# Kernel tuning notes

Hardware: AMD Instinct MI355X
Metric: run time of the kernel (lower is better)

## Reference

```python
import jax, jax.numpy as jnp
import numpy as np

TOP_K = 2

def setup_inputs() -> dict:
    key = jax.random.key(0)
    ks = jax.random.split(key, 5)
    B, S, H, F, E = 4, 512, 1024, 3584, 8
    x = jax.random.normal(ks[0], (B, S, H), dtype=jnp.float32)
    gate_w = jax.random.normal(ks[1], (H, E), dtype=jnp.float32) * (1.0 / np.sqrt(H))
    w1 = jax.random.normal(ks[2], (E, F, H), dtype=jnp.float32) * (1.0 / np.sqrt(H))
    w3 = jax.random.normal(ks[3], (E, F, H), dtype=jnp.float32) * (1.0 / np.sqrt(H))
    w2 = jax.random.normal(ks[4], (E, H, F), dtype=jnp.float32) * (1.0 / np.sqrt(F))
    return {"x": x, "gate_w": gate_w, "w1": w1, "w3": w3, "w2": w2}


def reference(x, gate_w, w1, w3, w2):
    # MoE top-2 routing (Mixtral-style), dense-dispatch formulation.
    B, S, H = x.shape
    E = gate_w.shape[1]
    xt = x.reshape(-1, H)                      # [T, H] flattened tokens
    T = xt.shape[0]
    logits = xt @ gate_w                       # [T, E] gate logits
    top_w, top_i = jax.lax.top_k(logits, TOP_K)    # [T, K]
    top_w = jax.nn.softmax(top_w, axis=-1)         # softmax over selected-k logits
    # combine[t, e] = routing weight of expert e for token t (0 if not selected)
    combine = jnp.zeros((T, E), dtype=xt.dtype)
    combine = combine.at[jnp.arange(T)[:, None], top_i].add(top_w)
    # SwiGLU experts: y_e = w2_e @ (silu(w1_e x) * (w3_e x))
    h = jnp.einsum('th,efh->tef', xt, w1)      # [T, E, F]
    g = jnp.einsum('th,efh->tef', xt, w3)      # [T, E, F]
    act = jax.nn.silu(h) * g                   # [T, E, F]
    out_e = jnp.einsum('tef,ehf->teh', act, w2)  # [T, E, H]
    out = jnp.einsum('teh,te->th', out_e, combine)  # weighted combine over experts
    return out.reshape(B, S, H)
```

## Files before the change

kernel.cpp:

```cpp
#include <hip/hip_runtime.h>
#include <hip/hip_bf16.h>
#include <stdint.h>

#define TOKENS 2048
#define HDIM 1024
#define FDIM 3584
#define NEXP 8
#define BK 32

typedef __attribute__((ext_vector_type(8))) short short8;
typedef __attribute__((ext_vector_type(4))) float floatx4;

#define AS1 __attribute__((address_space(1)))
#define AS3 __attribute__((address_space(3)))

__device__ __forceinline__ void glds16(const void* g, void* l) {
  __builtin_amdgcn_global_load_lds((const AS1 void*)g, (AS3 void*)l, 16, 0, 0);
}

__device__ __forceinline__ unsigned short f2bf(float f) {
  union { float f; unsigned int u; } c; c.f = f;
  unsigned int u = c.u;
  u += 0x7fffu + ((u >> 16) & 1u);
  return (unsigned short)(u >> 16);
}

__device__ __forceinline__ unsigned int pk2bf(float a, float b) {
  __hip_bfloat162 h = __float22bfloat162_rn(make_float2(a, b));
  union { __hip_bfloat162 h; unsigned int u; } c; c.h = h;
  return c.u;
}

__device__ __forceinline__ short8 pack_bf16(float4 c0, float4 c1) {
  union { short8 s; uint4 u; } o;
  o.u.x = pk2bf(c0.x, c0.y); o.u.y = pk2bf(c0.z, c0.w);
  o.u.z = pk2bf(c1.x, c1.y); o.u.w = pk2bf(c1.z, c1.w);
  return o.s;
}

__global__ void gate_kernel(const float* __restrict__ x,
                            const float* __restrict__ gw,
                            int* __restrict__ top_e,
                            float* __restrict__ top_w,
                            int* __restrict__ count) {
  int wv = threadIdx.x >> 6;
  int lane = threadIdx.x & 63;
  int t = blockIdx.x * 4 + wv;
  if (t >= TOKENS) return;
  float p[NEXP];
#pragma unroll
  for (int e = 0; e < NEXP; e++) p[e] = 0.f;
  const float* xr = x + (size_t)t * HDIM;
  for (int h = lane; h < HDIM; h += 64) {
    float xv = xr[h];
    const float4* g4 = (const float4*)(gw + (size_t)h * NEXP);
    float4 a = g4[0], b = g4[1];
    p[0] += xv * a.x; p[1] += xv * a.y; p[2] += xv * a.z; p[3] += xv * a.w;
    p[4] += xv * b.x; p[5] += xv * b.y; p[6] += xv * b.z; p[7] += xv * b.w;
  }
#pragma unroll
  for (int e = 0; e < NEXP; e++) {
#pragma unroll
    for (int off = 32; off > 0; off >>= 1) p[e] += __shfl_xor(p[e], off, 64);
  }
  if (lane == 0) {
    int i0 = 0;
    for (int e = 1; e < NEXP; e++) if (p[e] > p[i0]) i0 = e;
    int i1 = (i0 == 0) ? 1 : 0;
    for (int e = 0; e < NEXP; e++) if (e != i0 && p[e] > p[i1]) i1 = e;
    float l0 = p[i0], l1 = p[i1];
    float e1 = __expf(l1 - l0);
    float s = 1.f + e1;
    top_e[t * 2] = i0; top_e[t * 2 + 1] = i1;
    top_w[t * 2] = 1.f / s; top_w[t * 2 + 1] = e1 / s;
    atomicAdd(&count[i0], 1);
    atomicAdd(&count[i1], 1);
  }
}

__global__ void offsets_kernel(const int* __restrict__ count,
                               int* __restrict__ offs,
                               int* __restrict__ cursor) {
  if (threadIdx.x == 0 && blockIdx.x == 0) {
    int o = 0;
    for (int e = 0; e < NEXP; e++) { offs[e] = o; cursor[e] = o; o += count[e]; }
  }
}

__global__ void scatter_kernel(const int* __restrict__ top_e,
                               int* __restrict__ cursor,
                               int* __restrict__ tok_of,
                               int* __restrict__ slot_of) {
  int t = blockIdx.x * blockDim.x + threadIdx.x;
  if (t >= TOKENS) return;
#pragma unroll
  for (int k = 0; k < 2; k++) {
    int e = top_e[t * 2 + k];
    int g = atomicAdd(&cursor[e], 1);
    tok_of[g] = t;
    slot_of[t * 2 + k] = g;
  }
}

__global__ void xconv_kernel(const float* __restrict__ x,
                             unsigned short* __restrict__ xbf) {
  int i = (blockIdx.x * blockDim.x + threadIdx.x) * 4;
  float4 v = *(const float4*)(x + i);
  uint2 pk;
  pk.x = pk2bf(v.x, v.y);
  pk.y = pk2bf(v.z, v.w);
  *(uint2*)(xbf + i) = pk;
}

#define G1_BM 128
#define G1_BF 64

__global__ __launch_bounds__(256, 3)
void gemm1_kernel(const unsigned short* __restrict__ xbf,
                  const float* __restrict__ w1,
                  const float* __restrict__ w3,
                  const int* __restrict__ count,
                  const int* __restrict__ offs,
                  const int* __restrict__ tok_of,
                  unsigned short* __restrict__ act) {
  int e = blockIdx.z;
  int cnt = count[e];
  int m0 = blockIdx.y * G1_BM;
  if (m0 >= cnt) return;
  int f0 = blockIdx.x * G1_BF;
  int off_e = offs[e];

  __shared__ __align__(16) unsigned short sA[G1_BM * 32];
  __shared__ __align__(16) float sB1[G1_BF * 32];
  __shared__ __align__(16) float sB3[G1_BF * 32];

  int tid = threadIdx.x;
  int lane = tid & 63, wv = tid >> 6;

  const unsigned short* ag[2];
  char* alb[2];
  const float* g1p[2]; const float* g3p[2];
  char* blb[2];
#pragma unroll
  for (int p = 0; p < 2; p++) {
    int c = tid + p * 256;
    {
      int row = c >> 2, slot = c & 3;
      int gch = slot ^ ((row >> 1) & 3);
      int r = m0 + row;
      int tok = tok_of[off_e + (r < cnt ? r : 0)];
      ag[p] = xbf + (size_t)tok * HDIM + gch * 8;
      alb[p] = (char*)sA + (wv * 64 + p * 256) * 16;
    }
    {
      int row = c >> 3, slot = c & 7;
      int gch = slot ^ (row & 7);
      g1p[p] = w1 + ((size_t)e * FDIM + f0 + row) * HDIM + gch * 4;
      g3p[p] = w3 + ((size_t)e * FDIM + f0 + row) * HDIM + gch * 4;
      blb[p] = (char*)sB1 + (wv * 64 + p * 256) * 16;
    }
  }
  size_t b3delta = (char*)sB3 - (char*)sB1;

  int lrow = lane & 15, quad = lane >> 4;
  int wm = wv >> 1, wn = wv & 1;

  floatx4 acc1[4][2], acc3[4][2];
#pragma unroll
  for (int i = 0; i < 4; i++)
#pragma unroll
    for (int j = 0; j < 2; j++) {
      acc1[i][j] = (floatx4){0.f, 0.f, 0.f, 0.f};
      acc3[i][j] = (floatx4){0.f, 0.f, 0.f, 0.f};
    }

  for (int k0 = 0; k0 < HDIM; k0 += BK) {
    __syncthreads();
#pragma unroll
    for (int p = 0; p < 2; p++) {
      glds16(ag[p] + k0, alb[p]);
      glds16(g1p[p] + k0, blb[p]);
      glds16(g3p[p] + k0, blb[p] + b3delta);
    }
    __syncthreads();

    short8 af[4], b1f[2], b3f[2];
#pragma unroll
    for (int ms = 0; ms < 4; ms++) {
      int r = wm * 64 + ms * 16 + lrow;
      int sl = quad ^ ((r >> 1) & 3);
      af[ms] = *(const short8*)(sA + r * 32 + sl * 8);
    }
#pragma unroll
    for (int ns = 0; ns < 2; ns++) {
      int r = wn * 32 + ns * 16 + lrow;
      int s0 = (2 * quad) ^ (r & 7), s1 = (2 * quad + 1) ^ (r & 7);
      float4 c0 = *(const float4*)(sB1 + r * 32 + s0 * 4);
      float4 c1 = *(const float4*)(sB1 + r * 32 + s1 * 4);
      b1f[ns] = pack_bf16(c0, c1);
      float4 d0 = *(const float4*)(sB3 + r * 32 + s0 * 4);
      float4 d1 = *(const float4*)(sB3 + r * 32 + s1 * 4);
      b3f[ns] = pack_bf16(d0, d1);
    }
#pragma unroll
    for (int ms = 0; ms < 4; ms++)
#pragma unroll
      for (int ns = 0; ns < 2; ns++) {
        acc1[ms][ns] = __builtin_amdgcn_mfma_f32_16x16x32_bf16(af[ms], b1f[ns], acc1[ms][ns], 0, 0, 0);
        acc3[ms][ns] = __builtin_amdgcn_mfma_f32_16x16x32_bf16(af[ms], b3f[ns], acc3[ms][ns], 0, 0, 0);
      }
  }

#pragma unroll
  for (int ms = 0; ms < 4; ms++) {
#pragma unroll
    for (int reg = 0; reg < 4; reg++) {
      int slot = m0 + wm * 64 + ms * 16 + quad * 4 + reg;
      if (slot < cnt) {
        unsigned short* ar = act + (size_t)(off_e + slot) * FDIM + f0 + wn * 32;
#pragma unroll
        for (int ns = 0; ns < 2; ns++) {
          float h = acc1[ms][ns][reg];
          float g = acc3[ms][ns][reg];
          float a = h / (1.f + __expf(-h)) * g;
          ar[ns * 16 + lrow] = f2bf(a);
        }
      }
    }
  }
}

#define G2_BM 128
#define G2_BN 128
#define SPLITK 4
#define G2_KS (FDIM / SPLITK)

__global__ __launch_bounds__(256, 3)
void gemm2_kernel(const unsigned short* __restrict__ act,
                  const float* __restrict__ w2,
                  const int* __restrict__ count,
                  const int* __restrict__ offs,
                  float* __restrict__ part) {
  int zz = blockIdx.z;
  int e = zz & 7, sk = zz >> 3;
  int cnt = count[e];
  int m0 = blockIdx.y * G2_BM;
  if (m0 >= cnt) return;
  int h0 = blockIdx.x * G2_BN;
  int off_e = offs[e];
  int kb = sk * G2_KS;

  __shared__ __align__(16) unsigned short sA[G2_BM * 32];
  __shared__ __align__(16) float sB[G2_BN * 32];

  int tid = threadIdx.x;
  int lane = tid & 63, wv = tid >> 6;

  const unsigned short* ag[2];
  char* alb[2];
#pragma unroll
  for (int p = 0; p < 2; p++) {
    int c = tid + p * 256;
    int row = c >> 2, slot = c & 3;
    int gch = slot ^ ((row >> 1) & 3);
    int r = m0 + row;
    int rr = (r < cnt ? r : 0);
    ag[p] = act + (size_t)(off_e + rr) * FDIM + kb + gch * 8;
    alb[p] = (char*)sA + (wv * 64 + p * 256) * 16;
  }
  const float* bg[4];
  char* blb[4];
#pragma unroll
  for (int p = 0; p < 4; p++) {
    int c = tid + p * 256;
    int row = c >> 3, slot = c & 7;
    int gch = slot ^ (row & 7);
    bg[p] = w2 + ((size_t)e * HDIM + h0 + row) * FDIM + kb + gch * 4;
    blb[p] = (char*)sB + (wv * 64 + p * 256) * 16;
  }

  int lrow = lane & 15, quad = lane >> 4;
  int wm = wv >> 1, wn = wv & 1;

  floatx4 acc[4][4];
#pragma unroll
  for (int i = 0; i < 4; i++)
#pragma unroll
    for (int j = 0; j < 4; j++) acc[i][j] = (floatx4){0.f, 0.f, 0.f, 0.f};

  for (int k0 = 0; k0 < G2_KS; k0 += BK) {
    __syncthreads();
#pragma unroll
    for (int p = 0; p < 2; p++) glds16(ag[p] + k0, alb[p]);
#pragma unroll
    for (int p = 0; p < 4; p++) glds16(bg[p] + k0, blb[p]);
    __syncthreads();

    short8 af[4], bf[4];
#pragma unroll
    for (int ms = 0; ms < 4; ms++) {
      int r = wm * 64 + ms * 16 + lrow;
      int sl = quad ^ ((r >> 1) & 3);
      af[ms] = *(const short8*)(sA + r * 32 + sl * 8);
    }
#pragma unroll
    for (int ns = 0; ns < 4; ns++) {
      int r = wn * 64 + ns * 16 + lrow;
      int s0 = (2 * quad) ^ (r & 7), s1 = (2 * quad + 1) ^ (r & 7);
      float4 c0 = *(const float4*)(sB + r * 32 + s0 * 4);
      float4 c1 = *(const float4*)(sB + r * 32 + s1 * 4);
      bf[ns] = pack_bf16(c0, c1);
    }
#pragma unroll
    for (int ms = 0; ms < 4; ms++)
#pragma unroll
      for (int ns = 0; ns < 4; ns++)
        acc[ms][ns] = __builtin_amdgcn_mfma_f32_16x16x32_bf16(af[ms], bf[ns], acc[ms][ns], 0, 0, 0);
  }

#pragma unroll
  for (int ms = 0; ms < 4; ms++) {
#pragma unroll
    for (int reg = 0; reg < 4; reg++) {
      int slot = m0 + wm * 64 + ms * 16 + quad * 4 + reg;
      if (slot < cnt) {
        float* crow = part + ((size_t)sk * 4096 + off_e + slot) * HDIM + h0 + wn * 64;
#pragma unroll
        for (int ns = 0; ns < 4; ns++)
          crow[ns * 16 + lrow] = acc[ms][ns][reg];
      }
    }
  }
}

__global__ void combine_kernel(const float* __restrict__ part,
                               const int* __restrict__ slot_of,
                               const float* __restrict__ top_w,
                               float* __restrict__ out) {
  int t = blockIdx.x;
  int g0 = slot_of[t * 2], g1 = slot_of[t * 2 + 1];
  float w0 = top_w[t * 2], w1 = top_w[t * 2 + 1];
  int i = threadIdx.x;
  float4 s0 = {0.f, 0.f, 0.f, 0.f}, s1 = {0.f, 0.f, 0.f, 0.f};
#pragma unroll
  for (int sk = 0; sk < SPLITK; sk++) {
    float4 a = ((const float4*)(part + ((size_t)sk * 4096 + g0) * HDIM))[i];
    float4 b = ((const float4*)(part + ((size_t)sk * 4096 + g1) * HDIM))[i];
    s0.x += a.x; s0.y += a.y; s0.z += a.z; s0.w += a.w;
    s1.x += b.x; s1.y += b.y; s1.z += b.z; s1.w += b.w;
  }
  float4 r;
  r.x = w0 * s0.x + w1 * s1.x;
  r.y = w0 * s0.y + w1 * s1.y;
  r.z = w0 * s0.z + w1 * s1.z;
  r.w = w0 * s0.w + w1 * s1.w;
  ((float4*)(out + (size_t)t * HDIM))[i] = r;
}

extern "C" void kernel_launch(void* const* d_in, const int* in_sizes, int n_in,
                              void* d_out, int out_size, void* d_ws, size_t ws_size,
                              hipStream_t stream) {
  const float* x  = (const float*)d_in[0];
  const float* gw = (const float*)d_in[1];
  const float* w1 = (const float*)d_in[2];
  const float* w3 = (const float*)d_in[3];
  const float* w2 = (const float*)d_in[4];
  float* out = (float*)d_out;

  char* ws = (char*)d_ws;
  const size_t XBF_OFF = 0;
  const size_t ACT_OFF = 4ull << 20;
  const size_t PART_OFF = 36ull << 20;
  const size_t SML_OFF = 100ull << 20;

  unsigned short* xbf = (unsigned short*)(ws + XBF_OFF);
  unsigned short* act = (unsigned short*)(ws + ACT_OFF);
  float* part = (float*)(ws + PART_OFF);
  float* top_w = (float*)(ws + SML_OFF);
  int* top_e   = (int*)(ws + SML_OFF + 16384);
  int* slot_of = (int*)(ws + SML_OFF + 32768);
  int* tok_of  = (int*)(ws + SML_OFF + 49152);
  int* count   = (int*)(ws + SML_OFF + 65536);
  int* offs    = (int*)(ws + SML_OFF + 65536 + 32);
  int* cursor  = (int*)(ws + SML_OFF + 65536 + 64);

  hipMemsetAsync(count, 0, 96, stream);

  gate_kernel<<<TOKENS / 4, 256, 0, stream>>>(x, gw, top_e, top_w, count);
  offsets_kernel<<<1, 64, 0, stream>>>(count, offs, cursor);
  scatter_kernel<<<TOKENS / 256, 256, 0, stream>>>(top_e, cursor, tok_of, slot_of);
  xconv_kernel<<<(TOKENS * HDIM) / (256 * 4), 256, 0, stream>>>(x, xbf);
  gemm1_kernel<<<dim3(FDIM / G1_BF, TOKENS / G1_BM, NEXP), 256, 0, stream>>>(
      xbf, w1, w3, count, offs, tok_of, act);
  gemm2_kernel<<<dim3(HDIM / G2_BN, TOKENS / G2_BM, NEXP * SPLITK), 256, 0, stream>>>(
      act, w2, count, offs, part);
  combine_kernel<<<TOKENS, 256, 0, stream>>>(part, slot_of, top_w, out);
}
```

Measured before the change: 566.7 us.

## Pre-convert expert weights to bf16 and double-buffer LDS tiles in both GEMMs

Adds a pass on every call that converts w1, w3 and w2 from fp32 to bf16 in workspace. Both expert GEMMs then stream half as many bytes from the weights and skip the per-tile fp32-to-bf16 packing in their inner loops. The GEMM main loops are also restructured into two-stage LDS double buffering with a single barrier per K step, and launch bounds are raised to 4 blocks per CU. The trade-off is an extra full read and write of all weights each call, plus a larger workspace layout in which the partial-sum buffer reuses the w1/w3 bf16 region once those are no longer needed.

```diff
diff --git a/kernel.cpp b/kernel.cpp
--- a/kernel.cpp
+++ b/kernel.cpp
@@ -29,13 +29,6 @@
   __hip_bfloat162 h = __float22bfloat162_rn(make_float2(a, b));
   union { __hip_bfloat162 h; unsigned int u; } c; c.h = h;
   return c.u;
-}
-
-__device__ __forceinline__ short8 pack_bf16(float4 c0, float4 c1) {
-  union { short8 s; uint4 u; } o;
-  o.u.x = pk2bf(c0.x, c0.y); o.u.y = pk2bf(c0.z, c0.w);
-  o.u.z = pk2bf(c1.x, c1.y); o.u.w = pk2bf(c1.z, c1.w);
-  return o.s;
 }
 
 __global__ void gate_kernel(const float* __restrict__ x,
@@ -112,13 +105,36 @@
   *(uint2*)(xbf + i) = pk;
 }
 
+#define WELEMS 29360128
+#define WBLK (WELEMS / 2048)
+
+__global__ void wconv_kernel(const float* __restrict__ w1,
+                             const float* __restrict__ w3,
+                             const float* __restrict__ w2,
+                             unsigned short* __restrict__ w1b,
+                             unsigned short* __restrict__ w3b,
+                             unsigned short* __restrict__ w2b) {
+  int b = blockIdx.x;
+  const float* src; unsigned short* dst;
+  if (b < WBLK) { src = w1; dst = w1b; }
+  else if (b < 2 * WBLK) { src = w3; dst = w3b; b -= WBLK; }
+  else { src = w2; dst = w2b; b -= 2 * WBLK; }
+  size_t i = ((size_t)b * 256 + threadIdx.x) * 8;
+  float4 v0 = *(const float4*)(src + i);
+  float4 v1 = *(const float4*)(src + i + 4);
+  uint4 o;
+  o.x = pk2bf(v0.x, v0.y); o.y = pk2bf(v0.z, v0.w);
+  o.z = pk2bf(v1.x, v1.y); o.w = pk2bf(v1.z, v1.w);
+  *(uint4*)(dst + i) = o;
+}
+
 #define G1_BM 128
 #define G1_BF 64
 
-__global__ __launch_bounds__(256, 3)
+__global__ __launch_bounds__(256, 4)
 void gemm1_kernel(const unsigned short* __restrict__ xbf,
-                  const float* __restrict__ w1,
-                  const float* __restrict__ w3,
+                  const unsigned short* __restrict__ w1b,
+                  const unsigned short* __restrict__ w3b,
                   const int* __restrict__ count,
                   const int* __restrict__ offs,
                   const int* __restrict__ tok_of,
@@ -130,37 +146,30 @@
   int f0 = blockIdx.x * G1_BF;
   int off_e = offs[e];
 
-  __shared__ __align__(16) unsigned short sA[G1_BM * 32];
-  __shared__ __align__(16) float sB1[G1_BF * 32];
-  __shared__ __align__(16) float sB3[G1_BF * 32];
+  __shared__ __align__(16) unsigned short sA[2][G1_BM * 32];
+  __shared__ __align__(16) unsigned short sB1[2][G1_BF * 32];
+  __shared__ __align__(16) unsigned short sB3[2][G1_BF * 32];
 
   int tid = threadIdx.x;
   int lane = tid & 63, wv = tid >> 6;
 
   const unsigned short* ag[2];
-  char* alb[2];
-  const float* g1p[2]; const float* g3p[2];
-  char* blb[2];
 #pragma unroll
   for (int p = 0; p < 2; p++) {
     int c = tid + p * 256;
-    {
-      int row = c >> 2, slot = c & 3;
-      int gch = slot ^ ((row >> 1) & 3);
-      int r = m0 + row;
-      int tok = tok_of[off_e + (r < cnt ? r : 0)];
-      ag[p] = xbf + (size_t)tok * HDIM + gch * 8;
-      alb[p] = (char*)sA + (wv * 64 + p * 256) * 16;
-    }
-    {
-      int row = c >> 3, slot = c & 7;
-      int gch = slot ^ (row & 7);
-      g1p[p] = w1 + ((size_t)e * FDIM + f0 + row) * HDIM + gch * 4;
-      g3p[p] = w3 + ((size_t)e * FDIM + f0 + row) * HDIM + gch * 4;
-      blb[p] = (char*)sB1 + (wv * 64 + p * 256) * 16;
-    }
-  }
-  size_t b3delta = (char*)sB3 - (char*)sB1;
+    int row = c >> 2, slot = c & 3;
+    int gch = slot ^ ((row >> 1) & 3);
+    int r = m0 + row;
+    int tok = tok_of[off_e + (r < cnt ? r : 0)];
+    ag[p] = xbf + (size_t)tok * HDIM + gch * 8;
+  }
+  unsigned aoff = (unsigned)(wv * 64) * 16;
+
+  int brow = tid >> 2, bslot = tid & 3;
+  int bgch = bslot ^ ((brow >> 1) & 3);
+  const unsigned short* b1g = w1b + ((size_t)e * FDIM + f0 + brow) * HDIM + bgch * 8;
+  const unsigned short* b3g = w3b + ((size_t)e * FDIM + f0 + brow) * HDIM + bgch * 8;
+  unsigned boff = (unsigned)(wv * 64) * 16;
 
   int lrow = lane & 15, quad = lane >> 4;
   int wm = wv >> 1, wn = wv & 1;
@@ -174,33 +183,38 @@
       acc3[i][j] = (floatx4){0.f, 0.f, 0.f, 0.f};
     }
 
+#pragma unroll
+  for (int p = 0; p < 2; p++)
+    glds16(ag[p], (char*)sA[0] + aoff + p * 4096);
+  glds16(b1g, (char*)sB1[0] + boff);
+  glds16(b3g, (char*)sB3[0] + boff);
+  __syncthreads();
+
+  int cur = 0;
   for (int k0 = 0; k0 < HDIM; k0 += BK) {
-    __syncthreads();
-#pragma unroll
-    for (int p = 0; p < 2; p++) {
-      glds16(ag[p] + k0, alb[p]);
-      glds16(g1p[p] + k0, blb[p]);
-      glds16(g3p[p] + k0, blb[p] + b3delta);
-    }
-    __syncthreads();
+    int kn = k0 + BK;
+    if (kn < HDIM) {
+      int nxt = cur ^ 1;
+#pragma unroll
+      for (int p = 0; p < 2; p++)
+        glds16(ag[p] + kn, (char*)sA[nxt] + aoff + p * 4096);
+      glds16(b1g + kn, (char*)sB1[nxt] + boff);
+      glds16(b3g + kn, (char*)sB3[nxt] + boff);
+    }
 
     short8 af[4], b1f[2], b3f[2];
 #pragma unroll
     for (int ms = 0; ms < 4; ms++) {
       int r = wm * 64 + ms * 16 + lrow;
       int sl = quad ^ ((r >> 1) & 3);
-      af[ms] = *(const short8*)(sA + r * 32 + sl * 8);
+      af[ms] = *(const short8*)(sA[cur] + r * 32 + sl * 8);
     }
 #pragma unroll
     for (int ns = 0; ns < 2; ns++) {
       int r = wn * 32 + ns * 16 + lrow;
-      int s0 = (2 * quad) ^ (r & 7), s1 = (2 * quad + 1) ^ (r & 7);
-      float4 c0 = *(const float4*)(sB1 + r * 32 + s0 * 4);
-      float4 c1 = *(const float4*)(sB1 + r * 32 + s1 * 4);
-      b1f[ns] = pack_bf16(c0, c1);
-      float4 d0 = *(const float4*)(sB3 + r * 32 + s0 * 4);
-      float4 d1 = *(const float4*)(sB3 + r * 32 + s1 * 4);
-      b3f[ns] = pack_bf16(d0, d1);
+      int sl = quad ^ ((r >> 1) & 3);
+      b1f[ns] = *(const short8*)(sB1[cur] + r * 32 + sl * 8);
+      b3f[ns] = *(const short8*)(sB3[cur] + r * 32 + sl * 8);
     }
 #pragma unroll
     for (int ms = 0; ms < 4; ms++)
@@ -209,6 +223,8 @@
         acc1[ms][ns] = __builtin_amdgcn_mfma_f32_16x16x32_bf16(af[ms], b1f[ns], acc1[ms][ns], 0, 0, 0);
         acc3[ms][ns] = __builtin_amdgcn_mfma_f32_16x16x32_bf16(af[ms], b3f[ns], acc3[ms][ns], 0, 0, 0);
       }
+    __syncthreads();
+    cur ^= 1;
   }
 
 #pragma unroll
@@ -235,9 +251,9 @@
 #define SPLITK 4
 #define G2_KS (FDIM / SPLITK)
 
-__global__ __launch_bounds__(256, 3)
+__global__ __launch_bounds__(256, 4)
 void gemm2_kernel(const unsigned short* __restrict__ act,
-                  const float* __restrict__ w2,
+                  const unsigned short* __restrict__ w2b,
                   const int* __restrict__ count,
                   const int* __restrict__ offs,
                   float* __restrict__ part) {
@@ -250,34 +266,27 @@
   int off_e = offs[e];
   int kb = sk * G2_KS;
 
-  __shared__ __align__(16) unsigned short sA[G2_BM * 32];
-  __shared__ __align__(16) float sB[G2_BN * 32];
+  __shared__ __align__(16) unsigned short sA[2][G2_BM * 32];
+  __shared__ __align__(16) unsigned short sB[2][G2_BN * 32];
 
   int tid = threadIdx.x;
   int lane = tid & 63, wv = tid >> 6;
 
   const unsigned short* ag[2];
-  char* alb[2];
+  const unsigned short* bg[2];
 #pragma unroll
   for (int p = 0; p < 2; p++) {
     int c = tid + p * 256;
     int row = c >> 2, slot = c & 3;
     int gch = slot ^ ((row >> 1) & 3);
-    int r = m0 + row;
-    int rr = (r < cnt ? r : 0);
-    ag[p] = act + (size_t)(off_e + rr) * FDIM + kb + gch * 8;
-    alb[p] = (char*)sA + (wv * 64 + p * 256) * 16;
-  }
-  const float* bg[4];
-  char* blb[4];
-#pragma unroll
-  for (int p = 0; p < 4; p++) {
-    int c = tid + p * 256;
-    int row = c >> 3, slot = c & 7;
-    int gch = slot ^ (row & 7);
-    bg[p] = w2 + ((size_t)e * HDIM + h0 + row) * FDIM + kb + gch * 4;
-    blb[p] = (char*)sB + (wv * 64 + p * 256) * 16;
-  }
+    {
+      int r = m0 + row;
+      int rr = (r < cnt ? r : 0);
+      ag[p] = act + (size_t)(off_e + rr) * FDIM + kb + gch * 8;
+    }
+    bg[p] = w2b + ((size_t)e * HDIM + h0 + row) * FDIM + kb + gch * 8;
+  }
+  unsigned off16 = (unsigned)(wv * 64) * 16;
 
   int lrow = lane & 15, quad = lane >> 4;
   int wm = wv >> 1, wn = wv & 1;
@@ -288,34 +297,45 @@
 #pragma unroll
     for (int j = 0; j < 4; j++) acc[i][j] = (floatx4){0.f, 0.f, 0.f, 0.f};
 
+#pragma unroll
+  for (int p = 0; p < 2; p++) {
+    glds16(ag[p], (char*)sA[0] + off16 + p * 4096);
+    glds16(bg[p], (char*)sB[0] + off16 + p * 4096);
+  }
+  __syncthreads();
+
+  int cur = 0;
   for (int k0 = 0; k0 < G2_KS; k0 += BK) {
-    __syncthreads();
-#pragma unroll
-    for (int p = 0; p < 2; p++) glds16(ag[p] + k0, alb[p]);
-#pragma unroll
-    for (int p = 0; p < 4; p++) glds16(bg[p] + k0, blb[p]);
-    __syncthreads();
+    int kn = k0 + BK;
+    if (kn < G2_KS) {
+      int nxt = cur ^ 1;
+#pragma unroll
+      for (int p = 0; p < 2; p++) {
+        glds16(ag[p] + kn, (char*)sA[nxt] + off16 + p * 4096);
+        glds16(bg[p] + kn, (char*)sB[nxt] + off16 + p * 4096);
+      }
+    }
 
     short8 af[4], bf[4];
 #pragma unroll
     for (int ms = 0; ms < 4; ms++) {
       int r = wm * 64 + ms * 16 + lrow;
       int sl = quad ^ ((r >> 1) & 3);
-      af[ms] = *(const short8*)(sA + r * 32 + sl * 8);
+      af[ms] = *(const short8*)(sA[cur] + r * 32 + sl * 8);
     }
 #pragma unroll
     for (int ns = 0; ns < 4; ns++) {
       int r = wn * 64 + ns * 16 + lrow;
-      int s0 = (2 * quad) ^ (r & 7), s1 = (2 * quad + 1) ^ (r & 7);
-      float4 c0 = *(const float4*)(sB + r * 32 + s0 * 4);
-      float4 c1 = *(const float4*)(sB + r * 32 + s1 * 4);
-      bf[ns] = pack_bf16(c0, c1);
+      int sl = quad ^ ((r >> 1) & 3);
+      bf[ns] = *(const short8*)(sB[cur] + r * 32 + sl * 8);
     }
 #pragma unroll
     for (int ms = 0; ms < 4; ms++)
 #pragma unroll
       for (int ns = 0; ns < 4; ns++)
         acc[ms][ns] = __builtin_amdgcn_mfma_f32_16x16x32_bf16(af[ms], bf[ns], acc[ms][ns], 0, 0, 0);
+    __syncthreads();
+    cur ^= 1;
   }
 
 #pragma unroll
@@ -368,21 +388,20 @@
   float* out = (float*)d_out;
 
   char* ws = (char*)d_ws;
-  const size_t XBF_OFF = 0;
-  const size_t ACT_OFF = 4ull << 20;
-  const size_t PART_OFF = 36ull << 20;
-  const size_t SML_OFF = 100ull << 20;
-
-  unsigned short* xbf = (unsigned short*)(ws + XBF_OFF);
-  unsigned short* act = (unsigned short*)(ws + ACT_OFF);
-  float* part = (float*)(ws + PART_OFF);
-  float* top_w = (float*)(ws + SML_OFF);
-  int* top_e   = (int*)(ws + SML_OFF + 16384);
-  int* slot_of = (int*)(ws + SML_OFF + 32768);
-  int* tok_of  = (int*)(ws + SML_OFF + 49152);
-  int* count   = (int*)(ws + SML_OFF + 65536);
-  int* offs    = (int*)(ws + SML_OFF + 65536 + 32);
-  int* cursor  = (int*)(ws + SML_OFF + 65536 + 64);
+  unsigned short* w1bf = (unsigned short*)(ws + (36ull << 20));
+  unsigned short* w3bf = (unsigned short*)(ws + (92ull << 20));
+  unsigned short* w2bf = (unsigned short*)(ws + (148ull << 20));
+  unsigned short* act  = (unsigned short*)(ws + (204ull << 20));
+  unsigned short* xbf  = (unsigned short*)(ws + (232ull << 20));
+  float* part = (float*)(ws + (36ull << 20));
+  char* sml = ws + (236ull << 20);
+  float* top_w = (float*)sml;
+  int* top_e   = (int*)(sml + 16384);
+  int* slot_of = (int*)(sml + 32768);
+  int* tok_of  = (int*)(sml + 49152);
+  int* count   = (int*)(sml + 65536);
+  int* offs    = (int*)(sml + 65536 + 32);
+  int* cursor  = (int*)(sml + 65536 + 64);
 
   hipMemsetAsync(count, 0, 96, stream);
 
@@ -390,9 +409,10 @@
   offsets_kernel<<<1, 64, 0, stream>>>(count, offs, cursor);
   scatter_kernel<<<TOKENS / 256, 256, 0, stream>>>(top_e, cursor, tok_of, slot_of);
   xconv_kernel<<<(TOKENS * HDIM) / (256 * 4), 256, 0, stream>>>(x, xbf);
+  wconv_kernel<<<3 * WBLK, 256, 0, stream>>>(w1, w3, w2, w1bf, w3bf, w2bf);
   gemm1_kernel<<<dim3(FDIM / G1_BF, TOKENS / G1_BM, NEXP), 256, 0, stream>>>(
-      xbf, w1, w3, count, offs, tok_of, act);
+      xbf, w1bf, w3bf, count, offs, tok_of, act);
   gemm2_kernel<<<dim3(HDIM / G2_BN, TOKENS / G2_BM, NEXP * SPLITK), 256, 0, stream>>>(
-      act, w2, count, offs, part);
+      act, w2bf, count, offs, part);
   combine_kernel<<<TOKENS, 256, 0, stream>>>(part, slot_of, top_w, out);
 }
```

New measurement: 598.8 us. 1.06x slower.
